# Kernel optimization log

Measured on AMD Instinct MI355X. Metric: run time of the kernel, lower is better.

## Reference

```python
import jax, jax.numpy as jnp
import numpy as np

B, V, N, C, H = 4, 8, 256, 768, 12
DH = C // H
NEG = -1e9


def setup_inputs() -> dict:
    key = jax.random.key(0)
    k0, k1, k2, k3, k4, k5 = jax.random.split(key, 6)
    feats = jax.random.normal(k0, (B, V, N, C), dtype=jnp.float32)
    is_ref = jax.random.randint(k1, (B, V), 0, 2).astype(bool)
    # nn.MultiheadAttention params: packed in_proj (3C, C) + bias, out_proj Linear(C, C)
    w_qkv = jax.random.normal(k2, (3 * C, C), dtype=jnp.float32) * 0.02
    b_qkv = jax.random.normal(k3, (3 * C,), dtype=jnp.float32) * 0.02
    w_out = jax.random.normal(k4, (C, C), dtype=jnp.float32) * 0.02
    b_out = jax.random.normal(k5, (C,), dtype=jnp.float32) * 0.02
    return {"feats": feats, "is_ref": is_ref, "w_qkv": w_qkv, "b_qkv": b_qkv,
            "w_out": w_out, "b_out": b_out}


def reference(feats, is_ref, w_qkv, b_qkv, w_out, b_out):
    b_, v_, n_, c_ = feats.shape
    # packed QKV projection (torch Linear: x @ W.T + b)
    qkv = feats @ w_qkv.T + b_qkv                      # (B,V,N,3C)
    q, k, v = jnp.split(qkv, 3, axis=-1)
    q = q.reshape(b_, v_, n_, H, DH) * (1.0 / jnp.sqrt(jnp.float32(DH)))
    k = k.reshape(b_, v_ * n_, H, DH)                  # keys flattened over views
    v = v.reshape(b_, v_ * n_, H, DH)
    # view v attends to views w with opposite ref flag
    allowed = is_ref[:, :, None] ^ is_ref[:, None, :]  # (B,V,V) bool
    key_mask = jnp.repeat(allowed, n_, axis=2)         # (B,V,V*N)
    scores = jnp.einsum('bvnhd,bmhd->bhvnm', q, k)     # (B,H,V,N,V*N)
    logits = jnp.where(key_mask[:, None, :, None, :], scores, NEG)
    attn = jax.nn.softmax(logits, axis=-1)
    ctx = jnp.einsum('bhvnm,bmhd->bvnhd', attn, v).reshape(b_, v_, n_, c_)
    out = ctx @ w_out.T + b_out
    # views with empty context pass through unchanged
    has_ctx = allowed.any(axis=-1)                     # (B,V)
    return jnp.where(has_ctx[:, :, None, None], out, feats)
```

## Files before the change

kernel.cpp:

```cpp
#include <hip/hip_runtime.h>
#include <hip/hip_bf16.h>
#include <math.h>

#define BDIM 4
#define VDIM 8
#define NDIM 256
#define CDIM 768
#define HDIM 12
#define DHE  64
#define C3   (3*CDIM)
#define ROWS (BDIM*VDIM*NDIM)
#define KEYS (VDIM*NDIM)

typedef __attribute__((ext_vector_type(8))) short short8;
typedef __attribute__((ext_vector_type(4))) float float4v;

__device__ inline unsigned short f2bf(float f) {
    unsigned int u = __builtin_bit_cast(unsigned int, f);
    u += 0x7fffu + ((u >> 16) & 1u);
    return (unsigned short)(u >> 16);
}

__device__ __forceinline__ unsigned int pk2(float a, float b) {
    return (unsigned int)f2bf(a) | ((unsigned int)f2bf(b) << 16);
}

__device__ __forceinline__ uint4 pk8(float4 a, float4 b) {
    uint4 r;
    r.x = pk2(a.x, a.y); r.y = pk2(a.z, a.w);
    r.z = pk2(b.x, b.y); r.w = pk2(b.z, b.w);
    return r;
}

__device__ __forceinline__ void gld_lds16(const unsigned short* g, unsigned short* l) {
    __builtin_amdgcn_global_load_lds(
        (const __attribute__((address_space(1))) void*)g,
        (__attribute__((address_space(3))) void*)l, 16, 0, 0);
}

#define NA8 786432
#define NW8 221184
#define NO8 73728

__global__ __launch_bounds__(256) void cast_bf16_all(
    const float* __restrict__ fA, const float* __restrict__ fW,
    const float* __restrict__ fO,
    unsigned short* __restrict__ bA, unsigned short* __restrict__ bW,
    unsigned short* __restrict__ bO)
{
    const int gid = blockIdx.x * 256 + threadIdx.x;
    const float* src;
    unsigned short* dst;
    int idx;
    if (gid < NA8)            { src = fA; dst = bA; idx = gid; }
    else if (gid < NA8 + NW8) { src = fW; dst = bW; idx = gid - NA8; }
    else                      { src = fO; dst = bO; idx = gid - NA8 - NW8; }
    const float4* p = (const float4*)(src + (size_t)idx * 8);
    *(uint4*)(dst + (size_t)idx * 8) = pk8(p[0], p[1]);
}

__global__ __launch_bounds__(256) void gemm_qkv_mfma(
    const unsigned short* __restrict__ A,
    const unsigned short* __restrict__ W,
    const float* __restrict__ bias,
    unsigned short* __restrict__ out,
    unsigned short* __restrict__ vT)
{
    __shared__ __attribute__((aligned(16))) unsigned short As[2][128][32];
    __shared__ __attribute__((aligned(16))) unsigned short Ws[2][128][32];
    const int t = threadIdx.x;
    const int wave = t >> 6, lane = t & 63;
    const int m = lane & 15, quad = lane >> 4;
    const int wr = (wave >> 1) * 64, wc = (wave & 1) * 64;

    const int lin = blockIdx.y * gridDim.x + blockIdx.x;
    const int cpx = (gridDim.x * gridDim.y) >> 3;
    const int swz = (lin & 7) * cpx + (lin >> 3);
    const int row0 = (swz / gridDim.x) * 128, col0 = (swz % gridDim.x) * 128;

    const int sr = t >> 2, sk = (t & 3) * 8;
    const unsigned short* ag = &A[(size_t)(row0 + sr) * CDIM + sk];
    const unsigned short* wg = &W[(size_t)(col0 + sr) * CDIM + sk];

    float4v acc[4][4] = {};

    for (int k0 = 0; k0 < CDIM; k0 += 64) {
        #pragma unroll
        for (int ks = 0; ks < 2; ks++) {
            gld_lds16(ag + k0 + ks * 32, &As[ks][sr][sk]);
            gld_lds16(ag + (size_t)64 * CDIM + k0 + ks * 32, &As[ks][64 + sr][sk]);
            gld_lds16(wg + k0 + ks * 32, &Ws[ks][sr][sk]);
            gld_lds16(wg + (size_t)64 * CDIM + k0 + ks * 32, &Ws[ks][64 + sr][sk]);
        }
        __syncthreads();
        #pragma unroll
        for (int ks = 0; ks < 2; ks++) {
            short8 a[4], b[4];
            #pragma unroll
            for (int rt = 0; rt < 4; rt++)
                a[rt] = *(const short8*)&As[ks][wr + rt * 16 + m][quad * 8];
            #pragma unroll
            for (int ct = 0; ct < 4; ct++)
                b[ct] = *(const short8*)&Ws[ks][wc + ct * 16 + m][quad * 8];
            #pragma unroll
            for (int rt = 0; rt < 4; rt++)
                #pragma unroll
                for (int ct = 0; ct < 4; ct++)
                    acc[rt][ct] = __builtin_amdgcn_mfma_f32_16x16x32_bf16(
                        a[rt], b[ct], acc[rt][ct], 0, 0, 0);
        }
        __syncthreads();
    }

    if (col0 < 2 * CDIM) {
        #pragma unroll
        for (int ct = 0; ct < 4; ct++) {
            const int col = col0 + wc + ct * 16 + m;
            const float bv = bias[col];
            #pragma unroll
            for (int rt = 0; rt < 4; rt++) {
                const size_t row = (size_t)row0 + wr + rt * 16 + quad * 4;
                #pragma unroll
                for (int r = 0; r < 4; r++)
                    out[(row + r) * C3 + col] = f2bf(acc[rt][ct][r] + bv);
            }
        }
    } else {
        #pragma unroll
        for (int ct = 0; ct < 4; ct++) {
            const int vcol = col0 + wc + ct * 16 + m - 2 * CDIM;
            const int h = vcol >> 6, d = vcol & 63;
            const float bv = bias[col0 + wc + ct * 16 + m];
            #pragma unroll
            for (int rt = 0; rt < 4; rt++) {
                const int row = row0 + wr + rt * 16 + quad * 4;
                const int bidx = row >> 11, key = row & 2047;
                ushort4 pkv;
                pkv.x = f2bf(acc[rt][ct][0] + bv);
                pkv.y = f2bf(acc[rt][ct][1] + bv);
                pkv.z = f2bf(acc[rt][ct][2] + bv);
                pkv.w = f2bf(acc[rt][ct][3] + bv);
                *(ushort4*)&vT[((size_t)(bidx * HDIM + h) * DHE + d) * KEYS + key] = pkv;
            }
        }
    }
}

__global__ __launch_bounds__(256, 3) void attn_mfma(
    const unsigned short* __restrict__ qkv,
    const unsigned short* __restrict__ vT,
    const int* __restrict__ is_ref,
    unsigned short* __restrict__ ctx)
{
    const int g = blockIdx.x;
    const int myx = g & 7, cuu = (g >> 3) & 31, round = g >> 8;
    const int j = round * 32 + ((round & 1) ? (31 - cuu) : cuu);

    int rmask[4], r4[4];
    #pragma unroll
    for (int bb = 0; bb < 4; bb++) {
        int mask = 0;
        #pragma unroll
        for (int w = 0; w < VDIM; w++)
            if (is_ref[bb * VDIM + w] != 0) mask |= 1 << w;
        rmask[bb] = mask; r4[bb] = __popc(mask);
    }
    int ord[4] = {0, 1, 2, 3};
    #pragma unroll
    for (int i = 0; i < 3; i++)
        #pragma unroll
        for (int k = 0; k < 3 - i; k++) {
            const int wa = r4[ord[k]] * (8 - r4[ord[k]]);
            const int wb = r4[ord[k + 1]] * (8 - r4[ord[k + 1]]);
            if (wb > wa) { int tmp = ord[k]; ord[k] = ord[k + 1]; ord[k + 1] = tmp; }
        }
    int Gb[6], Gh[6], ng = 0;
    for (int p = 0; p < 48; p++) {
        const int row = p >> 3, col = p & 7;
        const int x = (row & 1) ? (7 - col) : col;
        if (x == myx) { Gb[ng] = ord[p / 12]; Gh[ng] = p % 12; ng++; }
    }
    int b = 0, h = 0, half = 0, v = 0, Lsel = 0;
    {
        int jj = j;
        bool found = false;
        for (int o = 8; o >= 0 && !found; o--) {
            for (int gi = 0; gi < 6 && !found; gi++) {
                const int b2 = Gb[gi], r2 = r4[b2];
                const int nv_o = ((8 - r2) == o ? r2 : 0) + (r2 == o ? (8 - r2) : 0);
                const int cnt = 2 * nv_o;
                if (cnt > 0 && jj < cnt) {
                    b = b2; h = Gh[gi]; Lsel = o;
                    half = jj / nv_o;
                    int pos = jj % nv_o;
                    int S = (((8 - r2) == o) ? rmask[b2] : 0)
                          | ((r2 == o) ? ((~rmask[b2]) & 0xff) : 0);
                    for (int vv = 0; vv < 8; vv++)
                        if ((S >> vv) & 1) { if (pos == 0) { v = vv; break; } pos--; }
                    found = true;
                } else jj -= cnt;
            }
        }
    }

    const int t = threadIdx.x, wave = t >> 6, lane = t & 63;
    const int m = lane & 15, quad = lane >> 4;
    const int n0 = half * 128 + wave * 32;

    __shared__ unsigned short Ks[128][64];
    __shared__ unsigned short Vs[64][128];
    __shared__ unsigned short Ps[4][32][72];

    const int my_ref = (rmask[b] >> v) & 1;
    const unsigned amask = my_ref ? (unsigned)((~rmask[b]) & 0xff)
                                  : (unsigned)rmask[b];
    const int nChunks = 2 * Lsel;

    const float c1 = 0.18033688f;

    short8 aq[2][2];
    #pragma unroll
    for (int qt = 0; qt < 2; qt++) {
        const size_t row = (size_t)((b * VDIM + v) * NDIM) + n0 + qt * 16 + m;
        #pragma unroll
        for (int ks = 0; ks < 2; ks++)
            aq[qt][ks] = *(const short8*)&qkv[row * C3 + h * DHE + ks * 32 + quad * 8];
    }

    float rs[2] = {0.f, 0.f};
    float4v O[2][4] = {};

    const int k_key = t >> 3, k_dg = t & 7;
    const int v_dim = t >> 4, v_kg = t & 15;

    const unsigned short* vTb = vT + (size_t)(b * HDIM + h) * DHE * KEYS;

    uint4 kreg[4], vreg[4];
    unsigned rem2 = amask;
    int wcur = __builtin_ffs((int)rem2) - 1;

    if (nChunks > 0) {
        const unsigned short* kb =
            qkv + (size_t)((b * VDIM + wcur) * NDIM) * C3 + CDIM + h * DHE;
        #pragma unroll
        for (int i = 0; i < 4; i++)
            kreg[i] = *(const uint4*)&kb[(size_t)(i * 32 + k_key) * C3 + k_dg * 8];
        #pragma unroll
        for (int i = 0; i < 4; i++)
            vreg[i] = *(const uint4*)&vTb[(size_t)(i * 16 + v_dim) * KEYS
                                          + wcur * NDIM + v_kg * 8];
    }

    for (int ci = 0; ci < nChunks; ci++) {
        __syncthreads();
        #pragma unroll
        for (int i = 0; i < 4; i++)
            *(uint4*)&Ks[i * 32 + k_key][(k_dg ^ (k_key & 7)) * 8] = kreg[i];
        #pragma unroll
        for (int i = 0; i < 4; i++)
            *(uint4*)&Vs[i * 16 + v_dim][(v_kg ^ v_dim) * 8] = vreg[i];

        if (ci + 1 < nChunks) {
            int wn, m0n;
            if ((ci & 1) == 0) { wn = wcur; m0n = 128; }
            else {
                unsigned r2 = rem2 & (rem2 - 1);
                wn = __builtin_ffs((int)r2) - 1; m0n = 0;
            }
            const unsigned short* kb =
                qkv + (size_t)((b * VDIM + wn) * NDIM + m0n) * C3 + CDIM + h * DHE;
            #pragma unroll
            for (int i = 0; i < 4; i++)
                kreg[i] = *(const uint4*)&kb[(size_t)(i * 32 + k_key) * C3 + k_dg * 8];
            #pragma unroll
            for (int i = 0; i < 4; i++)
                vreg[i] = *(const uint4*)&vTb[(size_t)(i * 16 + v_dim) * KEYS
                                              + wn * NDIM + m0n + v_kg * 8];
        }
        __syncthreads();

        #pragma unroll
        for (int hk = 0; hk < 2; hk++) {
            #pragma unroll
            for (int kt = 0; kt < 4; kt++) {
                const int nt = hk * 4 + kt;
                const short8 bk0 = *(const short8*)&Ks[nt * 16 + m][(quad ^ (m & 7)) * 8];
                const short8 bk1 = *(const short8*)&Ks[nt * 16 + m][((4 + quad) ^ (m & 7)) * 8];
                #pragma unroll
                for (int qt = 0; qt < 2; qt++) {
                    float4v s = {};
                    s = __builtin_amdgcn_mfma_f32_16x16x32_bf16(bk0, aq[qt][0], s, 0, 0, 0);
                    s = __builtin_amdgcn_mfma_f32_16x16x32_bf16(bk1, aq[qt][1], s, 0, 0, 0);
                    const float p0 = __builtin_amdgcn_exp2f(s[0] * c1);
                    const float p1 = __builtin_amdgcn_exp2f(s[1] * c1);
                    const float p2 = __builtin_amdgcn_exp2f(s[2] * c1);
                    const float p3 = __builtin_amdgcn_exp2f(s[3] * c1);
                    rs[qt] += (p0 + p1) + (p2 + p3);
                    uint2 pw;
                    pw.x = pk2(p0, p1);
                    pw.y = pk2(p2, p3);
                    *(uint2*)&Ps[wave][qt * 16 + m][kt * 16 + quad * 4] = pw;
                }
            }
            #pragma unroll
            for (int kk = 0; kk < 2; kk++) {
                const short8 ap0 = *(const short8*)&Ps[wave][m][kk * 32 + quad * 8];
                const short8 ap1 = *(const short8*)&Ps[wave][16 + m][kk * 32 + quad * 8];
                #pragma unroll
                for (int ct = 0; ct < 4; ct++) {
                    const short8 bv = *(const short8*)&Vs[ct * 16 + m]
                        [((hk * 8 + kk * 4 + quad) ^ m) * 8];
                    O[0][ct] = __builtin_amdgcn_mfma_f32_16x16x32_bf16(ap0, bv, O[0][ct], 0, 0, 0);
                    O[1][ct] = __builtin_amdgcn_mfma_f32_16x16x32_bf16(ap1, bv, O[1][ct], 0, 0, 0);
                }
            }
        }
        if (ci & 1) { rem2 &= rem2 - 1; wcur = __builtin_ffs((int)rem2) - 1; }
    }

    #pragma unroll
    for (int qt = 0; qt < 2; qt++) {
        float x = rs[qt];
        x += __shfl_xor(x, 16, 64);
        x += __shfl_xor(x, 32, 64);
        const float inv = (x > 0.f) ? 1.f / x : 0.f;
        float invq[4];
        #pragma unroll
        for (int r = 0; r < 4; r++)
            invq[r] = __shfl(inv, quad * 4 + r, 64);
        const size_t rowg = (size_t)((b * VDIM + v) * NDIM) + n0 + qt * 16 + quad * 4;
        #pragma unroll
        for (int ct = 0; ct < 4; ct++)
            #pragma unroll
            for (int r = 0; r < 4; r++)
                ctx[(rowg + r) * CDIM + h * DHE + ct * 16 + m] = f2bf(O[qt][ct][r] * invq[r]);
    }
}

__global__ __launch_bounds__(256) void gemm_out_mfma(
    const unsigned short* __restrict__ A,
    const unsigned short* __restrict__ W,
    const float* __restrict__ bias,
    const float* __restrict__ feats,
    const int* __restrict__ is_ref,
    float* __restrict__ out)
{
    __shared__ __attribute__((aligned(16))) unsigned short As[2][128][32];
    __shared__ __attribute__((aligned(16))) unsigned short Ws[2][128][32];
    const int t = threadIdx.x;
    const int wave = t >> 6, lane = t & 63;
    const int m = lane & 15, quad = lane >> 4;
    const int wr = (wave >> 1) * 64, wc = (wave & 1) * 64;

    const int lin = blockIdx.y * gridDim.x + blockIdx.x;
    const int cpx = (gridDim.x * gridDim.y) >> 3;
    const int swz = (lin & 7) * cpx + (lin >> 3);
    const int row0 = (swz / gridDim.x) * 128, col0 = (swz % gridDim.x) * 128;

    const int sr = t >> 2, sk = (t & 3) * 8;
    const unsigned short* ag = &A[(size_t)(row0 + sr) * CDIM + sk];
    const unsigned short* wg = &W[(size_t)(col0 + sr) * CDIM + sk];

    float4v acc[4][4] = {};

    for (int k0 = 0; k0 < CDIM; k0 += 64) {
        #pragma unroll
        for (int ks = 0; ks < 2; ks++) {
            gld_lds16(ag + k0 + ks * 32, &As[ks][sr][sk]);
            gld_lds16(ag + (size_t)64 * CDIM + k0 + ks * 32, &As[ks][64 + sr][sk]);
            gld_lds16(wg + k0 + ks * 32, &Ws[ks][sr][sk]);
            gld_lds16(wg + (size_t)64 * CDIM + k0 + ks * 32, &Ws[ks][64 + sr][sk]);
        }
        __syncthreads();
        #pragma unroll
        for (int ks = 0; ks < 2; ks++) {
            short8 a[4], b[4];
            #pragma unroll
            for (int rt = 0; rt < 4; rt++)
                a[rt] = *(const short8*)&As[ks][wr + rt * 16 + m][quad * 8];
            #pragma unroll
            for (int ct = 0; ct < 4; ct++)
                b[ct] = *(const short8*)&Ws[ks][wc + ct * 16 + m][quad * 8];
            #pragma unroll
            for (int rt = 0; rt < 4; rt++)
                #pragma unroll
                for (int ct = 0; ct < 4; ct++)
                    acc[rt][ct] = __builtin_amdgcn_mfma_f32_16x16x32_bf16(
                        a[rt], b[ct], acc[rt][ct], 0, 0, 0);
        }
        __syncthreads();
    }

    const int bidx = row0 / (VDIM * NDIM);
    const int vidx = (row0 / NDIM) % VDIM;
    const int my = is_ref[bidx * VDIM + vidx];
    bool has = false;
    #pragma unroll
    for (int w = 0; w < VDIM; w++) has = has || (is_ref[bidx * VDIM + w] != my);

    #pragma unroll
    for (int ct = 0; ct < 4; ct++) {
        const int col = col0 + wc + ct * 16 + m;
        const float bv = bias[col];
        #pragma unroll
        for (int rt = 0; rt < 4; rt++) {
            const size_t row = (size_t)row0 + wr + rt * 16 + quad * 4;
            #pragma unroll
            for (int r = 0; r < 4; r++) {
                float o = acc[rt][ct][r] + bv;
                if (!has) o = feats[(row + r) * CDIM + col];
                out[(row + r) * CDIM + col] = o;
            }
        }
    }
}

extern "C" void kernel_launch(void* const* d_in, const int* in_sizes, int n_in,
                              void* d_out, int out_size, void* d_ws, size_t ws_size,
                              hipStream_t stream) {
    const float* feats = (const float*)d_in[0];
    const int*   is_ref = (const int*)d_in[1];
    const float* w_qkv = (const float*)d_in[2];
    const float* b_qkv = (const float*)d_in[3];
    const float* w_out = (const float*)d_in[4];
    const float* b_out = (const float*)d_in[5];
    float* out = (float*)d_out;

    unsigned short* qkv_b = (unsigned short*)d_ws;
    unsigned short* vT    = qkv_b + (size_t)ROWS * C3;
    unsigned short* ctx_b = vT + (size_t)BDIM * HDIM * DHE * KEYS;
    unsigned short* A_bf  = ctx_b + (size_t)ROWS * CDIM;
    unsigned short* Wq_bf = A_bf + (size_t)ROWS * CDIM;
    unsigned short* Wo_bf = Wq_bf + (size_t)C3 * CDIM;

    cast_bf16_all<<<dim3((NA8 + NW8 + NO8) / 256), 256, 0, stream>>>(
        feats, w_qkv, w_out, A_bf, Wq_bf, Wo_bf);

    dim3 g1(C3 / 128, ROWS / 128);
    gemm_qkv_mfma<<<g1, 256, 0, stream>>>(A_bf, Wq_bf, b_qkv, qkv_b, vT);

    attn_mfma<<<dim3(768), 256, 0, stream>>>(qkv_b, vT, is_ref, ctx_b);

    dim3 g3(CDIM / 128, ROWS / 128);
    gemm_out_mfma<<<g3, 256, 0, stream>>>(ctx_b, Wo_bf, b_out, feats, is_ref, out);
    (void)in_sizes; (void)n_in; (void)out_size; (void)ws_size;
}
```

Baseline: 237.3 us.

## Double-buffer K/V LDS tiles with 64-key chunks and one barrier per chunk

Shrinks the attention K/V chunk from 128 to 64 keys and double-buffers the LDS tiles, so the next chunk is written to the alternate buffer while the current one is consumed. This drops one __syncthreads per iteration and lets global prefetch run two chunks ahead. Allowed view indices are precomputed into a packed nibble word instead of being walked with ffs on every step. The cost is twice as many iterations, with a barrier each, and a changed LDS swizzle for V.

```diff
diff --git a/kernel.cpp b/kernel.cpp
--- a/kernel.cpp
+++ b/kernel.cpp
@@ -207,14 +207,21 @@
     const int m = lane & 15, quad = lane >> 4;
     const int n0 = half * 128 + wave * 32;
 
-    __shared__ unsigned short Ks[128][64];
-    __shared__ unsigned short Vs[64][128];
+    __shared__ unsigned short Ks[2][64][64];
+    __shared__ unsigned short Vs[2][64][64];
     __shared__ unsigned short Ps[4][32][72];
 
     const int my_ref = (rmask[b] >> v) & 1;
     const unsigned amask = my_ref ? (unsigned)((~rmask[b]) & 0xff)
                                   : (unsigned)rmask[b];
-    const int nChunks = 2 * Lsel;
+    const int nC = 4 * Lsel;
+
+    unsigned vpack = 0;
+    {
+        unsigned rm = amask; int pi = 0;
+        while (rm) { vpack |= (unsigned)(__builtin_ffs((int)rm) - 1) << (4 * pi);
+                     rm &= rm - 1; pi++; }
+    }
 
     const float c1 = 0.18033688f;
 
@@ -230,93 +237,82 @@
     float rs[2] = {0.f, 0.f};
     float4v O[2][4] = {};
 
-    const int k_key = t >> 3, k_dg = t & 7;
-    const int v_dim = t >> 4, v_kg = t & 15;
+    const int s_row = t >> 2;
+    const int s_g   = (t & 3) * 2;
 
     const unsigned short* vTb = vT + (size_t)(b * HDIM + h) * DHE * KEYS;
-
-    uint4 kreg[4], vreg[4];
-    unsigned rem2 = amask;
-    int wcur = __builtin_ffs((int)rem2) - 1;
-
-    if (nChunks > 0) {
-        const unsigned short* kb =
-            qkv + (size_t)((b * VDIM + wcur) * NDIM) * C3 + CDIM + h * DHE;
-        #pragma unroll
-        for (int i = 0; i < 4; i++)
-            kreg[i] = *(const uint4*)&kb[(size_t)(i * 32 + k_key) * C3 + k_dg * 8];
-        #pragma unroll
-        for (int i = 0; i < 4; i++)
-            vreg[i] = *(const uint4*)&vTb[(size_t)(i * 16 + v_dim) * KEYS
-                                          + wcur * NDIM + v_kg * 8];
-    }
-
-    for (int ci = 0; ci < nChunks; ci++) {
+    const unsigned short* qkb = qkv + (size_t)(b * VDIM) * NDIM * C3 + CDIM + h * DHE;
+
+    uint4 kreg[2], vreg[2];
+
+    #define LOADC(c)                                                           \
+        {                                                                      \
+            const int w_ = (int)((vpack >> (((c) >> 2) * 4)) & 15);            \
+            const int kb_ = ((c) & 3) * 64;                                    \
+            const unsigned short* kp = qkb + (size_t)(w_ * NDIM + kb_ + s_row) * C3; \
+            kreg[0] = *(const uint4*)&kp[(s_g + 0) * 8];                       \
+            kreg[1] = *(const uint4*)&kp[(s_g + 1) * 8];                       \
+            const unsigned short* vp = vTb + (size_t)s_row * KEYS + w_ * NDIM + kb_; \
+            vreg[0] = *(const uint4*)&vp[(s_g + 0) * 8];                       \
+            vreg[1] = *(const uint4*)&vp[(s_g + 1) * 8];                       \
+        }
+    #define WRITEC(buf)                                                        \
+        {                                                                      \
+            *(uint4*)&Ks[buf][s_row][((s_g + 0) ^ (s_row & 7)) * 8] = kreg[0]; \
+            *(uint4*)&Ks[buf][s_row][((s_g + 1) ^ (s_row & 7)) * 8] = kreg[1]; \
+            *(uint4*)&Vs[buf][s_row][((s_g + 0) ^ (s_row & 7)) * 8] = vreg[0]; \
+            *(uint4*)&Vs[buf][s_row][((s_g + 1) ^ (s_row & 7)) * 8] = vreg[1]; \
+        }
+
+    if (nC > 0) {
+        LOADC(0);
+        WRITEC(0);
+        if (nC > 1) LOADC(1);
+    }
+
+    for (int c = 0; c < nC; c++) {
+        const int buf = c & 1;
         __syncthreads();
-        #pragma unroll
-        for (int i = 0; i < 4; i++)
-            *(uint4*)&Ks[i * 32 + k_key][(k_dg ^ (k_key & 7)) * 8] = kreg[i];
-        #pragma unroll
-        for (int i = 0; i < 4; i++)
-            *(uint4*)&Vs[i * 16 + v_dim][(v_kg ^ v_dim) * 8] = vreg[i];
-
-        if (ci + 1 < nChunks) {
-            int wn, m0n;
-            if ((ci & 1) == 0) { wn = wcur; m0n = 128; }
-            else {
-                unsigned r2 = rem2 & (rem2 - 1);
-                wn = __builtin_ffs((int)r2) - 1; m0n = 0;
-            }
-            const unsigned short* kb =
-                qkv + (size_t)((b * VDIM + wn) * NDIM + m0n) * C3 + CDIM + h * DHE;
-            #pragma unroll
-            for (int i = 0; i < 4; i++)
-                kreg[i] = *(const uint4*)&kb[(size_t)(i * 32 + k_key) * C3 + k_dg * 8];
-            #pragma unroll
-            for (int i = 0; i < 4; i++)
-                vreg[i] = *(const uint4*)&vTb[(size_t)(i * 16 + v_dim) * KEYS
-                                              + wn * NDIM + m0n + v_kg * 8];
-        }
-        __syncthreads();
-
-        #pragma unroll
-        for (int hk = 0; hk < 2; hk++) {
-            #pragma unroll
-            for (int kt = 0; kt < 4; kt++) {
-                const int nt = hk * 4 + kt;
-                const short8 bk0 = *(const short8*)&Ks[nt * 16 + m][(quad ^ (m & 7)) * 8];
-                const short8 bk1 = *(const short8*)&Ks[nt * 16 + m][((4 + quad) ^ (m & 7)) * 8];
-                #pragma unroll
-                for (int qt = 0; qt < 2; qt++) {
-                    float4v s = {};
-                    s = __builtin_amdgcn_mfma_f32_16x16x32_bf16(bk0, aq[qt][0], s, 0, 0, 0);
-                    s = __builtin_amdgcn_mfma_f32_16x16x32_bf16(bk1, aq[qt][1], s, 0, 0, 0);
-                    const float p0 = __builtin_amdgcn_exp2f(s[0] * c1);
-                    const float p1 = __builtin_amdgcn_exp2f(s[1] * c1);
-                    const float p2 = __builtin_amdgcn_exp2f(s[2] * c1);
-                    const float p3 = __builtin_amdgcn_exp2f(s[3] * c1);
-                    rs[qt] += (p0 + p1) + (p2 + p3);
-                    uint2 pw;
-                    pw.x = pk2(p0, p1);
-                    pw.y = pk2(p2, p3);
-                    *(uint2*)&Ps[wave][qt * 16 + m][kt * 16 + quad * 4] = pw;
-                }
-            }
-            #pragma unroll
-            for (int kk = 0; kk < 2; kk++) {
-                const short8 ap0 = *(const short8*)&Ps[wave][m][kk * 32 + quad * 8];
-                const short8 ap1 = *(const short8*)&Ps[wave][16 + m][kk * 32 + quad * 8];
-                #pragma unroll
-                for (int ct = 0; ct < 4; ct++) {
-                    const short8 bv = *(const short8*)&Vs[ct * 16 + m]
-                        [((hk * 8 + kk * 4 + quad) ^ m) * 8];
-                    O[0][ct] = __builtin_amdgcn_mfma_f32_16x16x32_bf16(ap0, bv, O[0][ct], 0, 0, 0);
-                    O[1][ct] = __builtin_amdgcn_mfma_f32_16x16x32_bf16(ap1, bv, O[1][ct], 0, 0, 0);
-                }
-            }
-        }
-        if (ci & 1) { rem2 &= rem2 - 1; wcur = __builtin_ffs((int)rem2) - 1; }
-    }
+        if (c + 1 < nC) {
+            WRITEC(buf ^ 1);
+            if (c + 2 < nC) LOADC(c + 2);
+        }
+
+        #pragma unroll
+        for (int kt = 0; kt < 4; kt++) {
+            const short8 bk0 = *(const short8*)&Ks[buf][kt * 16 + m][(quad ^ (m & 7)) * 8];
+            const short8 bk1 = *(const short8*)&Ks[buf][kt * 16 + m][((4 + quad) ^ (m & 7)) * 8];
+            #pragma unroll
+            for (int qt = 0; qt < 2; qt++) {
+                float4v s = {};
+                s = __builtin_amdgcn_mfma_f32_16x16x32_bf16(bk0, aq[qt][0], s, 0, 0, 0);
+                s = __builtin_amdgcn_mfma_f32_16x16x32_bf16(bk1, aq[qt][1], s, 0, 0, 0);
+                const float p0 = __builtin_amdgcn_exp2f(s[0] * c1);
+                const float p1 = __builtin_amdgcn_exp2f(s[1] * c1);
+                const float p2 = __builtin_amdgcn_exp2f(s[2] * c1);
+                const float p3 = __builtin_amdgcn_exp2f(s[3] * c1);
+                rs[qt] += (p0 + p1) + (p2 + p3);
+                uint2 pw;
+                pw.x = pk2(p0, p1);
+                pw.y = pk2(p2, p3);
+                *(uint2*)&Ps[wave][qt * 16 + m][kt * 16 + quad * 4] = pw;
+            }
+        }
+        #pragma unroll
+        for (int kk = 0; kk < 2; kk++) {
+            const short8 ap0 = *(const short8*)&Ps[wave][m][kk * 32 + quad * 8];
+            const short8 ap1 = *(const short8*)&Ps[wave][16 + m][kk * 32 + quad * 8];
+            #pragma unroll
+            for (int ct = 0; ct < 4; ct++) {
+                const short8 bv = *(const short8*)&Vs[buf][ct * 16 + m]
+                    [((kk * 4 + quad) ^ (m & 7)) * 8];
+                O[0][ct] = __builtin_amdgcn_mfma_f32_16x16x32_bf16(ap0, bv, O[0][ct], 0, 0, 0);
+                O[1][ct] = __builtin_amdgcn_mfma_f32_16x16x32_bf16(ap1, bv, O[1][ct], 0, 0, 0);
+            }
+        }
+    }
+    #undef LOADC
+    #undef WRITEC
 
     #pragma unroll
     for (int qt = 0; qt < 2; qt++) {
```

Measured after the change: 226.8 us. 4.4% less time.
